# Kernel tuning notes

Hardware: AMD Instinct MI355X
Metric: run time of the kernel (lower is better)

## Reference

```python
import jax, jax.numpy as jnp
import numpy as np

N = 8192      # batch_size * length
B = 8
K = 30
D = 320       # hidden_nf = input_nf = output_nf
EPS = 1e-8
DIST_W = 1.0


def setup_inputs() -> dict:
    key = jax.random.key(0)
    k1, k2, k3, k4, k5, k6, k7 = jax.random.split(key, 7)
    h = jax.random.normal(k1, (N, D), dtype=jnp.float32)
    coord = jax.random.normal(k2, (N, 3), dtype=jnp.float32)
    # row: each node repeated K times (fixed-k neighborhood grouping implied by reshape(B,-1,K))
    row = jnp.repeat(jnp.arange(N, dtype=jnp.int64), K)
    col = jax.random.randint(k3, (N * K,), 0, N, dtype=jnp.int64)
    edge_index = jnp.stack([row, col], axis=0)
    # node_mlp params: Linear(2D -> D), SiLU, Linear(D -> D)
    s1 = 1.0 / np.sqrt(2 * D)
    s2 = 1.0 / np.sqrt(D)
    W1 = jax.random.uniform(k4, (2 * D, D), jnp.float32, -s1, s1)
    b1 = jax.random.uniform(k5, (D,), jnp.float32, -s1, s1)
    W2 = jax.random.uniform(k6, (D, D), jnp.float32, -s2, s2)
    b2 = jax.random.uniform(k7, (D,), jnp.float32, -s2, s2)
    return {"h": h, "coord": coord, "W1": W1, "b1": b1, "W2": W2, "b2": b2,
            "edge_index": edge_index, "batch_size": B, "k": K}


def reference(h, coord, W1, b1, W2, b2, edge_index, batch_size, k):
    row, col = edge_index[0], edge_index[1]
    d = h.shape[-1]
    # coord2radial (normalize=False)
    coord_diff = coord[row] - coord[col]                      # [E,3]
    radial = jnp.sum(coord_diff ** 2, axis=1, keepdims=True)  # [E,1]
    # edge_model: dot-product attention fused with inverse-distance score
    src, tgt = h[row], h[col]                                 # [E,D]
    attn = jnp.sum(src * tgt, axis=-1).reshape(batch_size, -1, k)   # [B,L,K]
    dist_score = (1.0 / (radial + EPS)).reshape(batch_size, -1, k)  # [B,L,K]
    attn_score = jax.nn.softmax(attn + DIST_W * dist_score, axis=-1)[..., None]  # [B,L,K,1]
    edge_feat = tgt.reshape(batch_size, -1, k, d) * attn_score       # [B,L,K,D]
    # coord_model (coords_agg='mean')
    trans = coord_diff.reshape(batch_size, -1, k, 3) * attn_score    # [B,L,K,3]
    coord_out = coord + jnp.mean(trans, axis=2).reshape(-1, 3)
    # node_model (residual=True)
    agg = jnp.sum(edge_feat, axis=2).reshape(-1, d)                  # [N,D]
    z = jnp.concatenate([h, agg], axis=1)                            # [N,2D]
    out = jax.nn.silu(z @ W1 + b1) @ W2 + b2
    h_out = h + out
    return (h_out, coord_out)
```

## Files before the change

kernel.cpp:

```cpp
#include <hip/hip_runtime.h>
#include <hip/hip_bf16.h>
#include <math.h>

#define DHID 320
#define KNN  30

typedef float f4    __attribute__((ext_vector_type(4)));
typedef float f32x4 __attribute__((ext_vector_type(4)));
typedef short bf16x8 __attribute__((ext_vector_type(8)));
typedef short bf16x4 __attribute__((ext_vector_type(4)));

static __device__ __forceinline__ short f2bf(float x) {
    union { float f; unsigned u; } v; v.f = x;
    unsigned r = v.u + 0x7FFFu + ((v.u >> 16) & 1u);
    return (short)(r >> 16);
}

__global__ __launch_bounds__(256)
void edge_kernel(const float* __restrict__ h,
                 const float* __restrict__ coord,
                 const int*   __restrict__ col,
                 short*       __restrict__ aggb,
                 float*       __restrict__ coord_out,
                 int N)
{
    int wid  = (int)((blockIdx.x * 256u + threadIdx.x) >> 6);
    int lane = threadIdx.x & 63;
    if (wid >= N) return;

    const float* hi = h + (size_t)wid * DHID;
    f4    hv = *(const f4*)(hi + 4 * lane);
    float ht = hi[256 + lane];

    float cx = coord[3 * wid + 0];
    float cy = coord[3 * wid + 1];
    float cz = coord[3 * wid + 2];

    const int* cp = col + (size_t)wid * KNN;
    int jv = (lane < KNN) ? cp[lane] : 0;

    float run_m = -INFINITY, run_l = 0.f;
    f4    accv = {0.f, 0.f, 0.f, 0.f};
    float acct = 0.f;
    float ax = 0.f, ay = 0.f, az = 0.f;

#pragma unroll 2
    for (int k = 0; k < KNN; ++k) {
        int j = __shfl(jv, k);
        const float* hj = h + (size_t)j * DHID;
        f4    gv = *(const f4*)(hj + 4 * lane);
        float gt = hj[256 + lane];

        float dot = hv[0] * gv[0];
        dot = fmaf(hv[1], gv[1], dot);
        dot = fmaf(hv[2], gv[2], dot);
        dot = fmaf(hv[3], gv[3], dot);
        dot = fmaf(ht, gt, dot);
#pragma unroll
        for (int off = 32; off; off >>= 1) dot += __shfl_xor(dot, off);

        float dx = cx - coord[3 * j + 0];
        float dy = cy - coord[3 * j + 1];
        float dz = cz - coord[3 * j + 2];
        float radial = dx * dx + dy * dy + dz * dz;
        float s = dot + 1.0f / (radial + 1e-8f);

        float nm = fmaxf(run_m, s);
        float sc = __expf(run_m - nm);
        float w  = __expf(s - nm);
        run_l = run_l * sc + w;
        accv  = accv * sc + w * gv;
        acct  = acct * sc + w * gt;
        ax = ax * sc + w * dx;
        ay = ay * sc + w * dy;
        az = az * sc + w * dz;
        run_m = nm;
    }

    float inv = 1.0f / run_l;
    short* ao = aggb + (size_t)wid * DHID;
    bf16x4 o;
#pragma unroll
    for (int i = 0; i < 4; ++i) o[i] = f2bf(accv[i] * inv);
    *(bf16x4*)(ao + 4 * lane) = o;
    ao[256 + lane] = f2bf(acct * inv);

    if (lane == 0) {
        float s = inv / (float)KNN;
        coord_out[3 * wid + 0] = cx + ax * s;
        coord_out[3 * wid + 1] = cy + ay * s;
        coord_out[3 * wid + 2] = cz + az * s;
    }
}

__global__ __launch_bounds__(256)
void wconv_kernel(const float* __restrict__ W1, const float* __restrict__ W2,
                  short* __restrict__ Wt1, short* __restrict__ Wt2)
{
    int i = blockIdx.x * 256 + threadIdx.x;
    if (i < 640 * 320) {
        int k = i / 320, c = i - k * 320;
        Wt1[c * 640 + k] = f2bf(W1[i]);
    } else {
        int j = i - 640 * 320;
        int k = j / 320, c = j - k * 320;
        Wt2[c * 320 + k] = f2bf(W2[j]);
    }
}

__global__ __launch_bounds__(256)
void mlp_mfma_kernel(const float* __restrict__ h,
                     const short* __restrict__ aggb,
                     const short* __restrict__ Wt1,
                     const short* __restrict__ Wt2,
                     const float* __restrict__ b1,
                     const float* __restrict__ b2,
                     float*       __restrict__ hout)
{
    __shared__ short h1s[16 * DHID];

    const int tid  = threadIdx.x;
    const int lane = tid & 63;
    const int wv   = tid >> 6;
    const int lrow = lane & 15;
    const int kg   = lane >> 4;
    const int r0   = blockIdx.x * 16;
    const int c0   = wv * 5;

    f32x4 acc[5] = {};

    const float* hA = h    + (size_t)(r0 + lrow) * DHID + kg * 8;
    const short* gA = aggb + (size_t)(r0 + lrow) * DHID + kg * 8;
    const short* bB1 = Wt1 + kg * 8;

    for (int t = 0; t < 10; ++t) {
        f4 lo = *(const f4*)(hA + t * 32);
        f4 hi = *(const f4*)(hA + t * 32 + 4);
        bf16x8 a;
#pragma unroll
        for (int j = 0; j < 4; ++j) { a[j] = f2bf(lo[j]); a[4 + j] = f2bf(hi[j]); }
#pragma unroll
        for (int c = 0; c < 5; ++c) {
            bf16x8 b = *(const bf16x8*)(bB1 + (size_t)((c0 + c) * 16 + lrow) * 640 + t * 32);
            acc[c] = __builtin_amdgcn_mfma_f32_16x16x32_bf16(a, b, acc[c], 0, 0, 0);
        }
    }
    for (int t = 0; t < 10; ++t) {
        bf16x8 a = *(const bf16x8*)(gA + t * 32);
#pragma unroll
        for (int c = 0; c < 5; ++c) {
            bf16x8 b = *(const bf16x8*)(bB1 + (size_t)((c0 + c) * 16 + lrow) * 640 + (t + 10) * 32);
            acc[c] = __builtin_amdgcn_mfma_f32_16x16x32_bf16(a, b, acc[c], 0, 0, 0);
        }
    }

#pragma unroll
    for (int c = 0; c < 5; ++c) {
        int colc = (c0 + c) * 16 + lrow;
        float bb = b1[colc];
#pragma unroll
        for (int r = 0; r < 4; ++r) {
            int row = kg * 4 + r;
            float x = acc[c][r] + bb;
            x = x / (1.f + __expf(-x));
            h1s[row * DHID + (colc ^ ((row & 7) << 3))] = f2bf(x);
        }
    }
    __syncthreads();

    f32x4 acc2[5] = {};
    const short* bB2 = Wt2 + kg * 8;
    const char*  h1base = (const char*)h1s + lrow * (DHID * 2);
    const int    swz = (lrow & 7) << 4;

    for (int t = 0; t < 10; ++t) {
        bf16x8 a = *(const bf16x8*)(h1base + ((t * 64 + kg * 16) ^ swz));
#pragma unroll
        for (int c = 0; c < 5; ++c) {
            bf16x8 b = *(const bf16x8*)(bB2 + (size_t)((c0 + c) * 16 + lrow) * 320 + t * 32);
            acc2[c] = __builtin_amdgcn_mfma_f32_16x16x32_bf16(a, b, acc2[c], 0, 0, 0);
        }
    }

#pragma unroll
    for (int c = 0; c < 5; ++c) {
        int colc = (c0 + c) * 16 + lrow;
        float bb = b2[colc];
#pragma unroll
        for (int r = 0; r < 4; ++r) {
            int grow = r0 + kg * 4 + r;
            hout[(size_t)grow * DHID + colc] =
                acc2[c][r] + bb + h[(size_t)grow * DHID + colc];
        }
    }
}

extern "C" void kernel_launch(void* const* d_in, const int* in_sizes, int n_in,
                              void* d_out, int out_size, void* d_ws, size_t ws_size,
                              hipStream_t stream)
{
    const float* h     = (const float*)d_in[0];
    const float* coord = (const float*)d_in[1];
    const float* W1    = (const float*)d_in[2];
    const float* b1    = (const float*)d_in[3];
    const float* W2    = (const float*)d_in[4];
    const float* b2    = (const float*)d_in[5];
    const int*   ei    = (const int*)d_in[6];

    const int N  = in_sizes[0] / DHID;
    const int NK = N * KNN;

    float* out       = (float*)d_out;
    float* hout      = out;
    float* coord_out = out + (size_t)N * DHID;

    short* aggb = (short*)d_ws;
    short* Wt1  = aggb + (size_t)N * DHID;
    short* Wt2  = Wt1 + 320 * 640;

    const int* col = ei + NK;

    wconv_kernel<<<(640 * 320 + 320 * 320) / 256, 256, 0, stream>>>(W1, W2, Wt1, Wt2);
    edge_kernel<<<N / 4, 256, 0, stream>>>(h, coord, col, aggb, coord_out, N);
    mlp_mfma_kernel<<<N / 16, 256, 0, stream>>>(h, aggb, Wt1, Wt2, b1, b2, hout);
}
```

Baseline: 167.2 us.

## Pre-tile weights for MFMA, split MLP into two grid kernels, shuffle neighbor coords

The bf16 weight conversion now writes W1 and W2 in a tiled layout that matches the MFMA B-operand access, so each lane reads 16 contiguous bytes instead of striding across rows. When the workspace is large enough, the MLP is split into two kernels over a 2D grid with one 16-column output tile per wave. The input row tile is staged in swizzled LDS and the hidden activations go through a bf16 global buffer; otherwise a fused 320-thread fallback is used. The edge kernel also loads neighbor coordinates once per lane and broadcasts them by shuffle instead of doing a dependent gather every iteration. The split adds an extra launch and an h1 round trip through global memory.

New measurement: 139.1 us. -16.8%, faster.

```diff
diff --git a/kernel.cpp b/kernel.cpp
--- a/kernel.cpp
+++ b/kernel.cpp
@@ -38,6 +38,12 @@
 
     const int* cp = col + (size_t)wid * KNN;
     int jv = (lane < KNN) ? cp[lane] : 0;
+    float pjx = 0.f, pjy = 0.f, pjz = 0.f;
+    if (lane < KNN) {
+        pjx = coord[3 * jv + 0];
+        pjy = coord[3 * jv + 1];
+        pjz = coord[3 * jv + 2];
+    }
 
     float run_m = -INFINITY, run_l = 0.f;
     f4    accv = {0.f, 0.f, 0.f, 0.f};
@@ -59,9 +65,9 @@
 #pragma unroll
         for (int off = 32; off; off >>= 1) dot += __shfl_xor(dot, off);
 
-        float dx = cx - coord[3 * j + 0];
-        float dy = cy - coord[3 * j + 1];
-        float dz = cz - coord[3 * j + 2];
+        float dx = cx - __shfl(pjx, k);
+        float dy = cy - __shfl(pjy, k);
+        float dz = cz - __shfl(pjz, k);
         float radial = dx * dx + dy * dy + dz * dz;
         float s = dot + 1.0f / (radial + 1e-8f);
 
@@ -100,24 +106,26 @@
     int i = blockIdx.x * 256 + threadIdx.x;
     if (i < 640 * 320) {
         int k = i / 320, c = i - k * 320;
-        Wt1[c * 640 + k] = f2bf(W1[i]);
+        int tile = c >> 4, lr = c & 15;
+        int t = k >> 5, kg = (k >> 3) & 3, j = k & 7;
+        Wt1[(size_t)tile * (20 * 512) + t * 512 + kg * 128 + lr * 8 + j] = f2bf(W1[i]);
     } else {
-        int j = i - 640 * 320;
-        int k = j / 320, c = j - k * 320;
-        Wt2[c * 320 + k] = f2bf(W2[j]);
+        int q = i - 640 * 320;
+        int k = q / 320, c = q - k * 320;
+        int tile = c >> 4, lr = c & 15;
+        int t = k >> 5, kg = (k >> 3) & 3, j = k & 7;
+        Wt2[(size_t)tile * (10 * 512) + t * 512 + kg * 128 + lr * 8 + j] = f2bf(W2[q]);
     }
 }
 
 __global__ __launch_bounds__(256)
-void mlp_mfma_kernel(const float* __restrict__ h,
-                     const short* __restrict__ aggb,
-                     const short* __restrict__ Wt1,
-                     const short* __restrict__ Wt2,
-                     const float* __restrict__ b1,
-                     const float* __restrict__ b2,
-                     float*       __restrict__ hout)
-{
-    __shared__ short h1s[16 * DHID];
+void mlp1_kernel(const float* __restrict__ h,
+                 const short* __restrict__ aggb,
+                 const short* __restrict__ Wt1,
+                 const float* __restrict__ b1,
+                 short*       __restrict__ h1)
+{
+    __shared__ short zs[16 * 640];
 
     const int tid  = threadIdx.x;
     const int lane = tid & 63;
@@ -125,72 +133,185 @@
     const int lrow = lane & 15;
     const int kg   = lane >> 4;
     const int r0   = blockIdx.x * 16;
-    const int c0   = wv * 5;
-
-    f32x4 acc[5] = {};
-
-    const float* hA = h    + (size_t)(r0 + lrow) * DHID + kg * 8;
-    const short* gA = aggb + (size_t)(r0 + lrow) * DHID + kg * 8;
-    const short* bB1 = Wt1 + kg * 8;
-
+    const int tile = blockIdx.y * 4 + wv;
+
+    for (int c = tid; c < 1280; c += 256) {
+        int row = c / 80;
+        int zc  = (c - row * 80) * 8;
+        int sw  = (row & 7) << 4;
+        bf16x8 v;
+        if (zc < DHID) {
+            const float* hp = h + (size_t)(r0 + row) * DHID + zc;
+            f4 lo = *(const f4*)hp;
+            f4 hi = *(const f4*)(hp + 4);
+#pragma unroll
+            for (int j = 0; j < 4; ++j) { v[j] = f2bf(lo[j]); v[4 + j] = f2bf(hi[j]); }
+        } else {
+            v = *(const bf16x8*)(aggb + (size_t)(r0 + row) * DHID + (zc - DHID));
+        }
+        *(bf16x8*)((char*)zs + ((row * 1280 + zc * 2) ^ sw)) = v;
+    }
+    __syncthreads();
+
+    const int   sw    = (lrow & 7) << 4;
+    const char* abase = (const char*)zs + lrow * 1280;
+    const short* B    = Wt1 + (size_t)tile * (20 * 512) + kg * 128 + lrow * 8;
+
+    f32x4 acc = {};
+#pragma unroll 5
+    for (int t = 0; t < 20; ++t) {
+        bf16x8 a = *(const bf16x8*)(abase + ((t * 64 + kg * 16) ^ sw));
+        bf16x8 b = *(const bf16x8*)(B + t * 512);
+        acc = __builtin_amdgcn_mfma_f32_16x16x32_bf16(a, b, acc, 0, 0, 0);
+    }
+
+    int   colc = tile * 16 + lrow;
+    float bb   = b1[colc];
+#pragma unroll
+    for (int r = 0; r < 4; ++r) {
+        int grow = r0 + kg * 4 + r;
+        float x = acc[r] + bb;
+        x = x / (1.f + __expf(-x));
+        h1[(size_t)grow * DHID + colc] = f2bf(x);
+    }
+}
+
+__global__ __launch_bounds__(256)
+void mlp2_kernel(const float* __restrict__ h,
+                 const short* __restrict__ h1,
+                 const short* __restrict__ Wt2,
+                 const float* __restrict__ b2,
+                 float*       __restrict__ hout)
+{
+    __shared__ short hs[16 * 320];
+
+    const int tid  = threadIdx.x;
+    const int lane = tid & 63;
+    const int wv   = tid >> 6;
+    const int lrow = lane & 15;
+    const int kg   = lane >> 4;
+    const int r0   = blockIdx.x * 16;
+    const int tile = blockIdx.y * 4 + wv;
+
+    for (int c = tid; c < 640; c += 256) {
+        int row = c / 40;
+        int zc  = (c - row * 40) * 8;
+        int sw  = (row & 7) << 4;
+        bf16x8 v = *(const bf16x8*)(h1 + (size_t)(r0 + row) * DHID + zc);
+        *(bf16x8*)((char*)hs + ((row * 640 + zc * 2) ^ sw)) = v;
+    }
+    __syncthreads();
+
+    const int   sw    = (lrow & 7) << 4;
+    const char* abase = (const char*)hs + lrow * 640;
+    const short* B    = Wt2 + (size_t)tile * (10 * 512) + kg * 128 + lrow * 8;
+
+    f32x4 acc = {};
+#pragma unroll 5
     for (int t = 0; t < 10; ++t) {
-        f4 lo = *(const f4*)(hA + t * 32);
-        f4 hi = *(const f4*)(hA + t * 32 + 4);
-        bf16x8 a;
-#pragma unroll
-        for (int j = 0; j < 4; ++j) { a[j] = f2bf(lo[j]); a[4 + j] = f2bf(hi[j]); }
-#pragma unroll
-        for (int c = 0; c < 5; ++c) {
-            bf16x8 b = *(const bf16x8*)(bB1 + (size_t)((c0 + c) * 16 + lrow) * 640 + t * 32);
-            acc[c] = __builtin_amdgcn_mfma_f32_16x16x32_bf16(a, b, acc[c], 0, 0, 0);
-        }
-    }
-    for (int t = 0; t < 10; ++t) {
-        bf16x8 a = *(const bf16x8*)(gA + t * 32);
-#pragma unroll
-        for (int c = 0; c < 5; ++c) {
-            bf16x8 b = *(const bf16x8*)(bB1 + (size_t)((c0 + c) * 16 + lrow) * 640 + (t + 10) * 32);
-            acc[c] = __builtin_amdgcn_mfma_f32_16x16x32_bf16(a, b, acc[c], 0, 0, 0);
-        }
-    }
-
-#pragma unroll
-    for (int c = 0; c < 5; ++c) {
-        int colc = (c0 + c) * 16 + lrow;
+        bf16x8 a = *(const bf16x8*)(abase + ((t * 64 + kg * 16) ^ sw));
+        bf16x8 b = *(const bf16x8*)(B + t * 512);
+        acc = __builtin_amdgcn_mfma_f32_16x16x32_bf16(a, b, acc, 0, 0, 0);
+    }
+
+    int   colc = tile * 16 + lrow;
+    float bb   = b2[colc];
+#pragma unroll
+    for (int r = 0; r < 4; ++r) {
+        int grow = r0 + kg * 4 + r;
+        hout[(size_t)grow * DHID + colc] =
+            acc[r] + bb + h[(size_t)grow * DHID + colc];
+    }
+}
+
+__global__ __launch_bounds__(320)
+void mlp_fused_kernel(const float* __restrict__ h,
+                      const short* __restrict__ aggb,
+                      const short* __restrict__ Wt1,
+                      const short* __restrict__ Wt2,
+                      const float* __restrict__ b1,
+                      const float* __restrict__ b2,
+                      float*       __restrict__ hout)
+{
+    __shared__ short zs[16 * 640];
+    __shared__ short h1s[16 * 320];
+
+    const int tid  = threadIdx.x;
+    const int lane = tid & 63;
+    const int wv   = tid >> 6;
+    const int lrow = lane & 15;
+    const int kg   = lane >> 4;
+    const int r0   = blockIdx.x * 16;
+
+    for (int c = tid; c < 1280; c += 320) {
+        int row = c / 80;
+        int zc  = (c - row * 80) * 8;
+        int sw  = (row & 7) << 4;
+        bf16x8 v;
+        if (zc < DHID) {
+            const float* hp = h + (size_t)(r0 + row) * DHID + zc;
+            f4 lo = *(const f4*)hp;
+            f4 hi = *(const f4*)(hp + 4);
+#pragma unroll
+            for (int j = 0; j < 4; ++j) { v[j] = f2bf(lo[j]); v[4 + j] = f2bf(hi[j]); }
+        } else {
+            v = *(const bf16x8*)(aggb + (size_t)(r0 + row) * DHID + (zc - DHID));
+        }
+        *(bf16x8*)((char*)zs + ((row * 1280 + zc * 2) ^ sw)) = v;
+    }
+    __syncthreads();
+
+    const int   sw    = (lrow & 7) << 4;
+    const char* abase = (const char*)zs + lrow * 1280;
+
+    f32x4 acc[4] = {};
+    {
+        const short* B = Wt1 + (size_t)(wv * 4) * (20 * 512) + kg * 128 + lrow * 8;
+        for (int t = 0; t < 20; ++t) {
+            bf16x8 a = *(const bf16x8*)(abase + ((t * 64 + kg * 16) ^ sw));
+#pragma unroll
+            for (int i = 0; i < 4; ++i) {
+                bf16x8 b = *(const bf16x8*)(B + (size_t)i * (20 * 512) + t * 512);
+                acc[i] = __builtin_amdgcn_mfma_f32_16x16x32_bf16(a, b, acc[i], 0, 0, 0);
+            }
+        }
+    }
+#pragma unroll
+    for (int i = 0; i < 4; ++i) {
+        int colc = (wv * 4 + i) * 16 + lrow;
         float bb = b1[colc];
 #pragma unroll
         for (int r = 0; r < 4; ++r) {
             int row = kg * 4 + r;
-            float x = acc[c][r] + bb;
+            float x = acc[i][r] + bb;
             x = x / (1.f + __expf(-x));
-            h1s[row * DHID + (colc ^ ((row & 7) << 3))] = f2bf(x);
+            *(short*)((char*)h1s + ((row * 640 + colc * 2) ^ ((row & 7) << 4))) = f2bf(x);
         }
     }
     __syncthreads();
 
-    f32x4 acc2[5] = {};
-    const short* bB2 = Wt2 + kg * 8;
-    const char*  h1base = (const char*)h1s + lrow * (DHID * 2);
-    const int    swz = (lrow & 7) << 4;
-
-    for (int t = 0; t < 10; ++t) {
-        bf16x8 a = *(const bf16x8*)(h1base + ((t * 64 + kg * 16) ^ swz));
-#pragma unroll
-        for (int c = 0; c < 5; ++c) {
-            bf16x8 b = *(const bf16x8*)(bB2 + (size_t)((c0 + c) * 16 + lrow) * 320 + t * 32);
-            acc2[c] = __builtin_amdgcn_mfma_f32_16x16x32_bf16(a, b, acc2[c], 0, 0, 0);
-        }
-    }
-
-#pragma unroll
-    for (int c = 0; c < 5; ++c) {
-        int colc = (c0 + c) * 16 + lrow;
+    f32x4 acc2[4] = {};
+    {
+        const short* B = Wt2 + (size_t)(wv * 4) * (10 * 512) + kg * 128 + lrow * 8;
+        const char* a2base = (const char*)h1s + lrow * 640;
+        for (int t = 0; t < 10; ++t) {
+            bf16x8 a = *(const bf16x8*)(a2base + ((t * 64 + kg * 16) ^ sw));
+#pragma unroll
+            for (int i = 0; i < 4; ++i) {
+                bf16x8 b = *(const bf16x8*)(B + (size_t)i * (10 * 512) + t * 512);
+                acc2[i] = __builtin_amdgcn_mfma_f32_16x16x32_bf16(a, b, acc2[i], 0, 0, 0);
+            }
+        }
+    }
+#pragma unroll
+    for (int i = 0; i < 4; ++i) {
+        int colc = (wv * 4 + i) * 16 + lrow;
         float bb = b2[colc];
 #pragma unroll
         for (int r = 0; r < 4; ++r) {
             int grow = r0 + kg * 4 + r;
             hout[(size_t)grow * DHID + colc] =
-                acc2[c][r] + bb + h[(size_t)grow * DHID + colc];
+                acc2[i][r] + bb + h[(size_t)grow * DHID + colc];
         }
     }
 }
@@ -216,11 +337,23 @@
 
     short* aggb = (short*)d_ws;
     short* Wt1  = aggb + (size_t)N * DHID;
-    short* Wt2  = Wt1 + 320 * 640;
+    short* Wt2  = Wt1 + 20 * 20 * 512;
+    short* h1   = Wt2 + 20 * 10 * 512;
+
+    const size_t need_split =
+        ((size_t)N * DHID * 2  + 20 * 20 * 512 + 20 * 10 * 512)
+        * sizeof(short);
 
     const int* col = ei + NK;
 
     wconv_kernel<<<(640 * 320 + 320 * 320) / 256, 256, 0, stream>>>(W1, W2, Wt1, Wt2);
     edge_kernel<<<N / 4, 256, 0, stream>>>(h, coord, col, aggb, coord_out, N);
-    mlp_mfma_kernel<<<N / 16, 256, 0, stream>>>(h, aggb, Wt1, Wt2, b1, b2, hout);
-}
+
+    if (ws_size >= need_split) {
+        dim3 g(N / 16, 5);
+        mlp1_kernel<<<g, 256, 0, stream>>>(h, aggb, Wt1, b1, h1);
+        mlp2_kernel<<<g, 256, 0, stream>>>(h, h1, Wt2, b2, hout);
+    } else {
+        mlp_fused_kernel<<<N / 16, 320, 0, stream>>>(h, aggb, Wt1, Wt2, b1, b2, hout);
+    }
+}
```

## Pre-tile weights into MFMA fragment layout, stage Z in LDS, prefetch neighbor coords

Applied to the files above, without the earlier changes.

The weight conversion kernel now writes W1 and W2 in a tiled layout that matches the MFMA B-fragment pattern, so each lane's 16-byte weight load is contiguous across the wave. The MLP kernel first stages the concatenated [h, agg] row block as bf16 into swizzled shared memory, then runs the first GEMM from LDS. The edge kernel loads each neighbor's coordinates once per lane and shuffles them, replacing per-iteration scattered global loads. The kernel launch order is also swapped, with the edge kernel issued before the weight conversion. LDS use per block grows, which may reduce occupancy.

Result: faster. 135.3 us (-19.1%).

```diff
diff --git a/kernel.cpp b/kernel.cpp
--- a/kernel.cpp
+++ b/kernel.cpp
@@ -38,6 +38,12 @@
 
     const int* cp = col + (size_t)wid * KNN;
     int jv = (lane < KNN) ? cp[lane] : 0;
+    float pjx = 0.f, pjy = 0.f, pjz = 0.f;
+    if (lane < KNN) {
+        pjx = coord[3 * jv + 0];
+        pjy = coord[3 * jv + 1];
+        pjz = coord[3 * jv + 2];
+    }
 
     float run_m = -INFINITY, run_l = 0.f;
     f4    accv = {0.f, 0.f, 0.f, 0.f};
@@ -59,9 +65,9 @@
 #pragma unroll
         for (int off = 32; off; off >>= 1) dot += __shfl_xor(dot, off);
 
-        float dx = cx - coord[3 * j + 0];
-        float dy = cy - coord[3 * j + 1];
-        float dz = cz - coord[3 * j + 2];
+        float dx = cx - __shfl(pjx, k);
+        float dy = cy - __shfl(pjy, k);
+        float dz = cz - __shfl(pjz, k);
         float radial = dx * dx + dy * dy + dz * dz;
         float s = dot + 1.0f / (radial + 1e-8f);
 
@@ -100,24 +106,29 @@
     int i = blockIdx.x * 256 + threadIdx.x;
     if (i < 640 * 320) {
         int k = i / 320, c = i - k * 320;
-        Wt1[c * 640 + k] = f2bf(W1[i]);
+        int tile = c >> 4, lr = c & 15;
+        int t = k >> 5, kg = (k >> 3) & 3, j = k & 7;
+        Wt1[(size_t)tile * (20 * 512) + t * 512 + kg * 128 + lr * 8 + j] = f2bf(W1[i]);
     } else {
-        int j = i - 640 * 320;
-        int k = j / 320, c = j - k * 320;
-        Wt2[c * 320 + k] = f2bf(W2[j]);
+        int q = i - 640 * 320;
+        int k = q / 320, c = q - k * 320;
+        int tile = c >> 4, lr = c & 15;
+        int t = k >> 5, kg = (k >> 3) & 3, j = k & 7;
+        Wt2[(size_t)tile * (10 * 512) + t * 512 + kg * 128 + lr * 8 + j] = f2bf(W2[q]);
     }
 }
 
 __global__ __launch_bounds__(256)
-void mlp_mfma_kernel(const float* __restrict__ h,
-                     const short* __restrict__ aggb,
-                     const short* __restrict__ Wt1,
-                     const short* __restrict__ Wt2,
-                     const float* __restrict__ b1,
-                     const float* __restrict__ b2,
-                     float*       __restrict__ hout)
-{
-    __shared__ short h1s[16 * DHID];
+void mlp_fused_kernel(const float* __restrict__ h,
+                      const short* __restrict__ aggb,
+                      const short* __restrict__ Wt1,
+                      const short* __restrict__ Wt2,
+                      const float* __restrict__ b1,
+                      const float* __restrict__ b2,
+                      float*       __restrict__ hout)
+{
+    __shared__ short zs[16 * 640];
+    __shared__ short h1s[16 * 320];
 
     const int tid  = threadIdx.x;
     const int lane = tid & 63;
@@ -125,72 +136,78 @@
     const int lrow = lane & 15;
     const int kg   = lane >> 4;
     const int r0   = blockIdx.x * 16;
-    const int c0   = wv * 5;
+
+    for (int c = tid; c < 1280; c += 256) {
+        int row = c / 80;
+        int zc  = (c - row * 80) * 8;
+        int sw  = (row & 7) << 4;
+        bf16x8 v;
+        if (zc < DHID) {
+            const float* hp = h + (size_t)(r0 + row) * DHID + zc;
+            f4 lo = *(const f4*)hp;
+            f4 hi = *(const f4*)(hp + 4);
+#pragma unroll
+            for (int j = 0; j < 4; ++j) { v[j] = f2bf(lo[j]); v[4 + j] = f2bf(hi[j]); }
+        } else {
+            v = *(const bf16x8*)(aggb + (size_t)(r0 + row) * DHID + (zc - DHID));
+        }
+        *(bf16x8*)((char*)zs + ((row * 1280 + zc * 2) ^ sw)) = v;
+    }
+    __syncthreads();
+
+    const int   sw    = (lrow & 7) << 4;
+    const char* abase = (const char*)zs + lrow * 1280;
 
     f32x4 acc[5] = {};
-
-    const float* hA = h    + (size_t)(r0 + lrow) * DHID + kg * 8;
-    const short* gA = aggb + (size_t)(r0 + lrow) * DHID + kg * 8;
-    const short* bB1 = Wt1 + kg * 8;
-
-    for (int t = 0; t < 10; ++t) {
-        f4 lo = *(const f4*)(hA + t * 32);
-        f4 hi = *(const f4*)(hA + t * 32 + 4);
-        bf16x8 a;
-#pragma unroll
-        for (int j = 0; j < 4; ++j) { a[j] = f2bf(lo[j]); a[4 + j] = f2bf(hi[j]); }
-#pragma unroll
-        for (int c = 0; c < 5; ++c) {
-            bf16x8 b = *(const bf16x8*)(bB1 + (size_t)((c0 + c) * 16 + lrow) * 640 + t * 32);
-            acc[c] = __builtin_amdgcn_mfma_f32_16x16x32_bf16(a, b, acc[c], 0, 0, 0);
-        }
-    }
-    for (int t = 0; t < 10; ++t) {
-        bf16x8 a = *(const bf16x8*)(gA + t * 32);
-#pragma unroll
-        for (int c = 0; c < 5; ++c) {
-            bf16x8 b = *(const bf16x8*)(bB1 + (size_t)((c0 + c) * 16 + lrow) * 640 + (t + 10) * 32);
-            acc[c] = __builtin_amdgcn_mfma_f32_16x16x32_bf16(a, b, acc[c], 0, 0, 0);
-        }
-    }
-
-#pragma unroll
-    for (int c = 0; c < 5; ++c) {
-        int colc = (c0 + c) * 16 + lrow;
+    {
+        const short* B = Wt1 + (size_t)(wv * 5) * (20 * 512) + kg * 128 + lrow * 8;
+        for (int t = 0; t < 20; ++t) {
+            bf16x8 a = *(const bf16x8*)(abase + ((t * 64 + kg * 16) ^ sw));
+#pragma unroll
+            for (int i = 0; i < 5; ++i) {
+                bf16x8 b = *(const bf16x8*)(B + (size_t)i * (20 * 512) + t * 512);
+                acc[i] = __builtin_amdgcn_mfma_f32_16x16x32_bf16(a, b, acc[i], 0, 0, 0);
+            }
+        }
+    }
+
+#pragma unroll
+    for (int i = 0; i < 5; ++i) {
+        int colc = (wv * 5 + i) * 16 + lrow;
         float bb = b1[colc];
 #pragma unroll
         for (int r = 0; r < 4; ++r) {
             int row = kg * 4 + r;
-            float x = acc[c][r] + bb;
+            float x = acc[i][r] + bb;
             x = x / (1.f + __expf(-x));
-            h1s[row * DHID + (colc ^ ((row & 7) << 3))] = f2bf(x);
+            *(short*)((char*)h1s + ((row * 640 + colc * 2) ^ ((row & 7) << 4))) = f2bf(x);
         }
     }
     __syncthreads();
 
     f32x4 acc2[5] = {};
-    const short* bB2 = Wt2 + kg * 8;
-    const char*  h1base = (const char*)h1s + lrow * (DHID * 2);
-    const int    swz = (lrow & 7) << 4;
-
-    for (int t = 0; t < 10; ++t) {
-        bf16x8 a = *(const bf16x8*)(h1base + ((t * 64 + kg * 16) ^ swz));
-#pragma unroll
-        for (int c = 0; c < 5; ++c) {
-            bf16x8 b = *(const bf16x8*)(bB2 + (size_t)((c0 + c) * 16 + lrow) * 320 + t * 32);
-            acc2[c] = __builtin_amdgcn_mfma_f32_16x16x32_bf16(a, b, acc2[c], 0, 0, 0);
-        }
-    }
-
-#pragma unroll
-    for (int c = 0; c < 5; ++c) {
-        int colc = (c0 + c) * 16 + lrow;
+    {
+        const short* B = Wt2 + (size_t)(wv * 5) * (10 * 512) + kg * 128 + lrow * 8;
+        const char* a2base = (const char*)h1s + lrow * 640;
+        for (int t = 0; t < 10; ++t) {
+            bf16x8 a = *(const bf16x8*)(a2base + ((t * 64 + kg * 16) ^ sw));
+#pragma unroll
+            for (int i = 0; i < 5; ++i) {
+                bf16x8 b = *(const bf16x8*)(B + (size_t)i * (10 * 512) + t * 512);
+                acc2[i] = __builtin_amdgcn_mfma_f32_16x16x32_bf16(a, b, acc2[i], 0, 0, 0);
+            }
+        }
+    }
+
+#pragma unroll
+    for (int i = 0; i < 5; ++i) {
+        int colc = (wv * 5 + i) * 16 + lrow;
         float bb = b2[colc];
 #pragma unroll
         for (int r = 0; r < 4; ++r) {
             int grow = r0 + kg * 4 + r;
             hout[(size_t)grow * DHID + colc] =
-                acc2[c][r] + bb + h[(size_t)grow * DHID + colc];
+                acc2[i][r] + bb + h[(size_t)grow * DHID + colc];
         }
     }
 }
@@ -216,11 +233,11 @@
 
     short* aggb = (short*)d_ws;
     short* Wt1  = aggb + (size_t)N * DHID;
-    short* Wt2  = Wt1 + 320 * 640;
+    short* Wt2  = Wt1 + 20 * 20 * 512;
 
     const int* col = ei + NK;
 
+    edge_kernel<<<N / 4, 256, 0, stream>>>(h, coord, col, aggb, coord_out, N);
     wconv_kernel<<<(640 * 320 + 320 * 320) / 256, 256, 0, stream>>>(W1, W2, Wt1, Wt2);
-    edge_kernel<<<N / 4, 256, 0, stream>>>(h, coord, col, aggb, coord_out, N);
-    mlp_mfma_kernel<<<N / 16, 256, 0, stream>>>(h, aggb, Wt1, Wt2, b1, b2, hout);
-}
+    mlp_fused_kernel<<<N / 16, 256, 0, stream>>>(h, aggb, Wt1, Wt2, b1, b2, hout);
+}
```
